# Kernel optimization log

Hardware: AMD Instinct MI355X
Metric: run time of the kernel (lower is better)

Reference implementation:

```python
import jax, jax.numpy as jnp
import numpy as np

HIDDEN = 256
HEADS = 8
DK = HIDDEN // HEADS
BH = 16  # bias_h_size
N = 2048
B = 1


def setup_inputs() -> dict:
    key = jax.random.key(0)
    ks = jax.random.split(key, 20)
    s = 0.02
    inp = {
        "int_chain_label": jax.random.randint(ks[0], (N, N), 0, 2, dtype=jnp.int32),
        "dist_map": jax.random.uniform(ks[1], (N, N), dtype=jnp.float32),
        "contact_map": jax.random.uniform(ks[2], (N, N), dtype=jnp.float32),
        "q": jax.random.normal(ks[3], (B, N, HIDDEN), dtype=jnp.float32),
        "k": jax.random.normal(ks[4], (B, N, HIDDEN), dtype=jnp.float32),
        "v": jax.random.normal(ks[5], (B, N, HIDDEN), dtype=jnp.float32),
        # projections
        "Wq": jax.random.normal(ks[6], (HIDDEN, HIDDEN), dtype=jnp.float32) * s,
        "bq": jnp.zeros((HIDDEN,), jnp.float32),
        "Wk": jax.random.normal(ks[7], (HIDDEN, HIDDEN), dtype=jnp.float32) * s,
        "bk": jnp.zeros((HIDDEN,), jnp.float32),
        "Wv": jax.random.normal(ks[8], (HIDDEN, HIDDEN), dtype=jnp.float32) * s,
        "bv": jnp.zeros((HIDDEN,), jnp.float32),
        "Wo": jax.random.normal(ks[9], (HIDDEN, HIDDEN), dtype=jnp.float32) * s,
        "bo": jnp.zeros((HIDDEN,), jnp.float32),
        # distance bias MLP: Linear(2, BH) -> Linear(BH, 1)
        "Wd1": jax.random.normal(ks[10], (2, BH), dtype=jnp.float32) * 0.5,
        "bd1": jnp.zeros((BH,), jnp.float32),
        "Wd2": jax.random.normal(ks[11], (BH, 1), dtype=jnp.float32) * 0.5,
        "bd2": jnp.zeros((1,), jnp.float32),
        # contact bias MLP
        "Wc1": jax.random.normal(ks[12], (2, BH), dtype=jnp.float32) * 0.5,
        "bc1": jnp.zeros((BH,), jnp.float32),
        "Wc2": jax.random.normal(ks[13], (BH, 1), dtype=jnp.float32) * 0.5,
        "bc2": jnp.zeros((1,), jnp.float32),
    }
    return inp


def _pair_bias(mp, label_f, W1, b1, W2, b2):
    # stack(map, label) -> [N,N,2]; two linears (no nonlinearity in original) -> [N,N]
    x = jnp.stack((mp, label_f), axis=-1)
    h = x @ W1 + b1                      # [N,N,BH]
    return (h @ W2 + b2)[..., 0]          # [N,N]


def reference(int_chain_label, dist_map, contact_map, q, k, v,
              Wq, bq, Wk, bk, Wv, bv, Wo, bo,
              Wd1, bd1, Wd2, bd2, Wc1, bc1, Wc2, bc2):
    label_f = int_chain_label.astype(jnp.float32)
    bias = (_pair_bias(dist_map, label_f, Wd1, bd1, Wd2, bd2)
            + _pair_bias(contact_map, label_f, Wc1, bc1, Wc2, bc2))  # [N,N]
    bias = bias[None, None]  # [1,1,N,N] broadcast over batch, heads

    b, n, _ = q.shape
    scale = DK ** -0.5
    qh = (q @ Wq + bq).reshape(b, n, HEADS, DK).transpose(0, 2, 1, 3) * scale  # [B,H,N,D]
    kh = (k @ Wk + bk).reshape(b, n, HEADS, DK).transpose(0, 2, 1, 3)
    vh = (v @ Wv + bv).reshape(b, n, HEADS, DK).transpose(0, 2, 1, 3)

    scores = jnp.einsum('bhnd,bhmd->bhnm', qh, kh) + bias  # [B,H,N,N]
    attn = jax.nn.softmax(scores, axis=-1)
    out = jnp.einsum('bhnm,bhmd->bhnd', attn, vh)           # [B,H,N,D]
    out = out.transpose(0, 2, 1, 3).reshape(b, n, HEADS * DK)
    return out @ Wo + bo
```

## Files before the change

kernel.cpp:

```cpp
#include <hip/hip_runtime.h>
#include <hip/hip_bf16.h>

#define SN 2048
#define HD 256
#define NHEAD 8
#define DK 32
#define BH 16

typedef __bf16 bf16;
typedef __bf16 bf16x8 __attribute__((ext_vector_type(8)));
typedef __bf16 bf16x4 __attribute__((ext_vector_type(4)));
typedef float f32x4 __attribute__((ext_vector_type(4)));
typedef int i32x4 __attribute__((ext_vector_type(4)));

__global__ void __launch_bounds__(256) prep_wt_kernel(
    const float* __restrict__ Wq, const float* __restrict__ Wk,
    const float* __restrict__ Wv, const float* __restrict__ Wo,
    bf16* __restrict__ wt)
{
    __shared__ bf16 tile[32][HD + 8];
    int bid = blockIdx.x;
    int t = threadIdx.x;
    const float* W = bid == 0 ? Wq : bid == 1 ? Wk : bid == 2 ? Wv : Wo;
    bf16* Wt = wt + bid * HD * HD;
    for (int r0 = 0; r0 < HD; r0 += 32) {
        #pragma unroll
        for (int i = 0; i < 32; i++) tile[i][t] = (bf16)W[(r0 + i) * HD + t];
        __syncthreads();
        #pragma unroll
        for (int i = 0; i < 32; i++) Wt[t * HD + r0 + i] = tile[i][t];
        __syncthreads();
    }
}

template<bool AF32, int MODE, bool OUTF32>
__device__ __forceinline__ void gemm_body(
    const void* __restrict__ Ap, const bf16* __restrict__ Wt,
    const float* __restrict__ bias, void* __restrict__ outp, int bid)
{
    int wave = threadIdx.x >> 6, lane = threadIdx.x & 63;
    int g = lane >> 4, qi = lane & 15;
    int mblk = bid & 31, nblk = bid >> 5;
    int m0 = mblk * 64 + wave * 16, n0 = nblk * 32;
    f32x4 acc0 = {0.f, 0.f, 0.f, 0.f}, acc1 = {0.f, 0.f, 0.f, 0.f};
    const bf16* W0 = Wt + (n0 + qi) * HD + 8 * g;
    const bf16* W1 = W0 + 16 * HD;
    #pragma unroll
    for (int ks = 0; ks < 8; ks++) {
        bf16x8 a;
        if constexpr (AF32) {
            const float* Ar = (const float*)Ap + (m0 + qi) * HD + 8 * g + ks * 32;
            f32x4 lo = *(const f32x4*)Ar;
            f32x4 hi = *(const f32x4*)(Ar + 4);
            #pragma unroll
            for (int e = 0; e < 4; e++) { a[e] = (bf16)lo[e]; a[4 + e] = (bf16)hi[e]; }
        } else {
            a = *(const bf16x8*)((const bf16*)Ap + (m0 + qi) * HD + 8 * g + ks * 32);
        }
        bf16x8 b0 = *(const bf16x8*)(W0 + ks * 32);
        bf16x8 b1 = *(const bf16x8*)(W1 + ks * 32);
        acc0 = __builtin_amdgcn_mfma_f32_16x16x32_bf16(a, b0, acc0, 0, 0, 0);
        acc1 = __builtin_amdgcn_mfma_f32_16x16x32_bf16(a, b1, acc1, 0, 0, 0);
    }
    float bv0 = bias[n0 + qi], bv1 = bias[n0 + 16 + qi];
    if constexpr (MODE == 0) {
        if constexpr (OUTF32) {
            float* out = (float*)outp;
            #pragma unroll
            for (int r = 0; r < 4; r++) {
                int m = m0 + 4 * g + r;
                out[m * HD + n0 + qi]      = acc0[r] + bv0;
                out[m * HD + n0 + 16 + qi] = acc1[r] + bv1;
            }
        } else {
            bf16* out = (bf16*)outp;
            #pragma unroll
            for (int r = 0; r < 4; r++) {
                int m = m0 + 4 * g + r;
                out[m * HD + n0 + qi]      = (bf16)(acc0[r] + bv0);
                out[m * HD + n0 + 16 + qi] = (bf16)(acc1[r] + bv1);
            }
        }
    } else {
        bf16* out = (bf16*)outp;
        bf16x4 v0, v1;
        #pragma unroll
        for (int r = 0; r < 4; r++) { v0[r] = (bf16)(acc0[r] + bv0); v1[r] = (bf16)(acc1[r] + bv1); }
        *(bf16x4*)(out + (n0 + qi) * SN + m0 + 4 * g)      = v0;
        *(bf16x4*)(out + (n0 + 16 + qi) * SN + m0 + 4 * g) = v1;
    }
}

__global__ void __launch_bounds__(256) qkv_kernel(
    const float* __restrict__ q, const float* __restrict__ k, const float* __restrict__ v,
    const bf16* __restrict__ wt,
    const float* __restrict__ bq, const float* __restrict__ bk, const float* __restrict__ bv,
    bf16* __restrict__ qh, bf16* __restrict__ kh, bf16* __restrict__ vt)
{
    int w = blockIdx.y;
    if (w == 0)      gemm_body<true, 0, false>(q, wt,               bq, qh, blockIdx.x);
    else if (w == 1) gemm_body<true, 0, false>(k, wt + HD * HD,     bk, kh, blockIdx.x);
    else             gemm_body<true, 1, false>(v, wt + 2 * HD * HD, bv, vt, blockIdx.x);
}

__global__ void __launch_bounds__(256) oproj_kernel(
    const bf16* __restrict__ A, const bf16* __restrict__ wt3,
    const float* __restrict__ bo, float* __restrict__ out)
{
    gemm_body<false, 0, true>(A, wt3, bo, out, blockIdx.x);
}

__global__ void __launch_bounds__(128) attn_kernel(
    const bf16* __restrict__ qh, const bf16* __restrict__ kh,
    const bf16* __restrict__ vt,
    const int* __restrict__ label, const float* __restrict__ dist,
    const float* __restrict__ contact,
    const float* __restrict__ Wd1, const float* __restrict__ bd1,
    const float* __restrict__ Wd2, const float* __restrict__ bd2,
    const float* __restrict__ Wc1, const float* __restrict__ bc1,
    const float* __restrict__ Wc2, const float* __restrict__ bc2,
    bf16* __restrict__ aout)
{
    int wave = threadIdx.x >> 6, lane = threadIdx.x & 63;
    int g = lane >> 4, qi = lane & 15;
    int h = blockIdx.x >> 6, qb = blockIdx.x & 63;
    int q0 = qb * 32 + wave * 16;

    float ad = 0.f, bld = 0.f, dd = bd2[0];
    #pragma unroll
    for (int j = 0; j < BH; j++) {
        float w2 = Wd2[j];
        ad  += Wd1[j] * w2;
        bld += Wd1[BH + j] * w2;
        dd  += bd1[j] * w2;
    }
    float ac = 0.f, blc = 0.f, dc = bc2[0];
    #pragma unroll
    for (int j = 0; j < BH; j++) {
        float w2 = Wc2[j];
        ac  += Wc1[j] * w2;
        blc += Wc1[BH + j] * w2;
        dc  += bc1[j] * w2;
    }
    float bl = bld + blc, dl = dd + dc;

    __shared__ bf16 plds[2][16][72];
    bf16 (*P)[72] = plds[wave];

    bf16x8 qf = *(const bf16x8*)(qh + (q0 + qi) * HD + h * DK + 8 * g);
    const bf16* kp  = kh + h * DK + 8 * g;
    const bf16* v0p = vt + (h * DK + qi) * SN + 8 * g;
    const bf16* v1p = v0p + 16 * SN;
    const float* dp = dist    + (q0 + qi) * SN + 4 * g;
    const float* cp = contact + (q0 + qi) * SN + 4 * g;
    const int*   lp = label   + (q0 + qi) * SN + 4 * g;

    const float scale = 0.17677669529663687f;
    float m = -1e30f, lsum = 0.f;
    f32x4 o0 = {0.f, 0.f, 0.f, 0.f}, o1 = {0.f, 0.f, 0.f, 0.f};

    for (int kt = 0; kt < 32; kt++) {
        int key0 = kt * 64;
        bf16x8 kf0 = *(const bf16x8*)(kp + (key0 +  0 + qi) * HD);
        bf16x8 kf1 = *(const bf16x8*)(kp + (key0 + 16 + qi) * HD);
        bf16x8 kf2 = *(const bf16x8*)(kp + (key0 + 32 + qi) * HD);
        bf16x8 kf3 = *(const bf16x8*)(kp + (key0 + 48 + qi) * HD);
        f32x4 dv0 = *(const f32x4*)(dp + key0 +  0), dv1 = *(const f32x4*)(dp + key0 + 16);
        f32x4 dv2 = *(const f32x4*)(dp + key0 + 32), dv3 = *(const f32x4*)(dp + key0 + 48);
        f32x4 cv0 = *(const f32x4*)(cp + key0 +  0), cv1 = *(const f32x4*)(cp + key0 + 16);
        f32x4 cv2 = *(const f32x4*)(cp + key0 + 32), cv3 = *(const f32x4*)(cp + key0 + 48);
        i32x4 lv0 = *(const i32x4*)(lp + key0 +  0), lv1 = *(const i32x4*)(lp + key0 + 16);
        i32x4 lv2 = *(const i32x4*)(lp + key0 + 32), lv3 = *(const i32x4*)(lp + key0 + 48);
        f32x4 zero = {0.f, 0.f, 0.f, 0.f};
        f32x4 s0 = __builtin_amdgcn_mfma_f32_16x16x32_bf16(kf0, qf, zero, 0, 0, 0);
        f32x4 s1 = __builtin_amdgcn_mfma_f32_16x16x32_bf16(kf1, qf, zero, 0, 0, 0);
        f32x4 s2 = __builtin_amdgcn_mfma_f32_16x16x32_bf16(kf2, qf, zero, 0, 0, 0);
        f32x4 s3 = __builtin_amdgcn_mfma_f32_16x16x32_bf16(kf3, qf, zero, 0, 0, 0);
        float x[16];
        #pragma unroll
        for (int r = 0; r < 4; r++) {
            float b0 = ad * dv0[r] + ac * cv0[r] + bl * (float)lv0[r] + dl;
            float b1 = ad * dv1[r] + ac * cv1[r] + bl * (float)lv1[r] + dl;
            float b2 = ad * dv2[r] + ac * cv2[r] + bl * (float)lv2[r] + dl;
            float b3 = ad * dv3[r] + ac * cv3[r] + bl * (float)lv3[r] + dl;
            x[r]      = s0[r] * scale + b0;
            x[4 + r]  = s1[r] * scale + b1;
            x[8 + r]  = s2[r] * scale + b2;
            x[12 + r] = s3[r] * scale + b3;
        }
        float tm = x[0];
        #pragma unroll
        for (int i = 1; i < 16; i++) tm = fmaxf(tm, x[i]);
        tm = fmaxf(tm, __shfl_xor(tm, 16));
        tm = fmaxf(tm, __shfl_xor(tm, 32));
        float mnew = fmaxf(m, tm);
        float f = __expf(m - mnew);
        float ps = 0.f;
        #pragma unroll
        for (int i = 0; i < 16; i++) { x[i] = __expf(x[i] - mnew); ps += x[i]; }
        ps += __shfl_xor(ps, 16);
        ps += __shfl_xor(ps, 32);
        lsum = lsum * f + ps;
        m = mnew;
        #pragma unroll
        for (int r = 0; r < 4; r++) { o0[r] *= f; o1[r] *= f; }
        #pragma unroll
        for (int s = 0; s < 4; s++) {
            bf16x4 pv;
            #pragma unroll
            for (int r = 0; r < 4; r++) pv[r] = (bf16)x[s * 4 + r];
            *(bf16x4*)(&P[qi][16 * s + 4 * g]) = pv;
        }
        __syncthreads();
        bf16x4 pa0 = *(const bf16x4*)(&P[qi][8 * g]);
        bf16x4 pa1 = *(const bf16x4*)(&P[qi][8 * g + 4]);
        bf16x4 pa2 = *(const bf16x4*)(&P[qi][32 + 8 * g]);
        bf16x4 pa3 = *(const bf16x4*)(&P[qi][32 + 8 * g + 4]);
        bf16x8 pb0 = __builtin_shufflevector(pa0, pa1, 0, 1, 2, 3, 4, 5, 6, 7);
        bf16x8 pb1 = __builtin_shufflevector(pa2, pa3, 0, 1, 2, 3, 4, 5, 6, 7);
        bf16x8 va00 = *(const bf16x8*)(v0p + key0);
        bf16x8 va01 = *(const bf16x8*)(v0p + key0 + 32);
        bf16x8 va10 = *(const bf16x8*)(v1p + key0);
        bf16x8 va11 = *(const bf16x8*)(v1p + key0 + 32);
        o0 = __builtin_amdgcn_mfma_f32_16x16x32_bf16(va00, pb0, o0, 0, 0, 0);
        o0 = __builtin_amdgcn_mfma_f32_16x16x32_bf16(va01, pb1, o0, 0, 0, 0);
        o1 = __builtin_amdgcn_mfma_f32_16x16x32_bf16(va10, pb0, o1, 0, 0, 0);
        o1 = __builtin_amdgcn_mfma_f32_16x16x32_bf16(va11, pb1, o1, 0, 0, 0);
        __syncthreads();
    }
    float inv = 1.f / lsum;
    bf16x4 r0, r1;
    #pragma unroll
    for (int r = 0; r < 4; r++) { r0[r] = (bf16)(o0[r] * inv); r1[r] = (bf16)(o1[r] * inv); }
    *(bf16x4*)(aout + (q0 + qi) * HD + h * DK + 4 * g)      = r0;
    *(bf16x4*)(aout + (q0 + qi) * HD + h * DK + 16 + 4 * g) = r1;
}

extern "C" void kernel_launch(void* const* d_in, const int* in_sizes, int n_in,
                              void* d_out, int out_size, void* d_ws, size_t ws_size,
                              hipStream_t stream)
{
    static const int expect[22] = {
        SN * SN, SN * SN, SN * SN,
        SN * HD, SN * HD, SN * HD,
        HD * HD, HD, HD * HD, HD,
        HD * HD, HD, HD * HD, HD,
        2 * BH, BH, BH, 1,
        2 * BH, BH, BH, 1
    };
    if (n_in != 22) return;
    for (int i = 0; i < 22; i++) if (in_sizes[i] != expect[i]) return;

    const int*   label   = (const int*)  d_in[0];
    const float* dist    = (const float*)d_in[1];
    const float* contact = (const float*)d_in[2];
    const float* q  = (const float*)d_in[3];
    const float* k  = (const float*)d_in[4];
    const float* v  = (const float*)d_in[5];
    const float* Wq = (const float*)d_in[6];  const float* bq = (const float*)d_in[7];
    const float* Wk = (const float*)d_in[8];  const float* bk = (const float*)d_in[9];
    const float* Wv = (const float*)d_in[10]; const float* bv = (const float*)d_in[11];
    const float* Wo = (const float*)d_in[12]; const float* bo = (const float*)d_in[13];
    const float* Wd1 = (const float*)d_in[14]; const float* bd1 = (const float*)d_in[15];
    const float* Wd2 = (const float*)d_in[16]; const float* bd2 = (const float*)d_in[17];
    const float* Wc1 = (const float*)d_in[18]; const float* bc1 = (const float*)d_in[19];
    const float* Wc2 = (const float*)d_in[20]; const float* bc2 = (const float*)d_in[21];

    char* ws = (char*)d_ws;
    bf16* qh   = (bf16*)(ws);
    bf16* kh   = (bf16*)(ws + (1u << 20));
    bf16* vt   = (bf16*)(ws + (2u << 20));
    bf16* aout = (bf16*)(ws + (3u << 20));
    bf16* wt   = (bf16*)(ws + (4u << 20));

    prep_wt_kernel<<<dim3(4), 256, 0, stream>>>(Wq, Wk, Wv, Wo, wt);

    qkv_kernel<<<dim3(256, 3), 256, 0, stream>>>(q, k, v, wt, bq, bk, bv, qh, kh, vt);

    attn_kernel<<<dim3(512), 128, 0, stream>>>(
        qh, kh, vt, label, dist, contact,
        Wd1, bd1, Wd2, bd2, Wc1, bc1, Wc2, bc2, aout);

    oproj_kernel<<<dim3(256), 256, 0, stream>>>(aout, wt + 3 * HD * HD, bo, (float*)d_out);
}
```

Before: 248.1 us.

## Split attention over key chunks with a separate combine kernel

The attention kernel now splits the key range into four chunks per (head, query block), which raises the grid from 512 to 2048 blocks. Each block writes partial outputs plus its running max and sum to workspace, and a new combine kernel merges them with log-sum-exp weights. The intra-wave __syncthreads are replaced with compiler memory barriers, since each wave uses its own LDS slice. The weight prep kernel is spread over 32 blocks, and the max reduction becomes a tree. This adds an extra launch and traffic for the partial results, and relies on LDS ordering within a wave without an explicit barrier.

```diff
diff --git a/kernel.cpp b/kernel.cpp
--- a/kernel.cpp
+++ b/kernel.cpp
@@ -6,6 +6,8 @@
 #define NHEAD 8
 #define DK 32
 #define BH 16
+#define KCH 4
+#define KTILES 8
 
 typedef __bf16 bf16;
 typedef __bf16 bf16x8 __attribute__((ext_vector_type(8)));
@@ -19,18 +21,16 @@
     bf16* __restrict__ wt)
 {
     __shared__ bf16 tile[32][HD + 8];
-    int bid = blockIdx.x;
+    int mat = blockIdx.x >> 3, rc = blockIdx.x & 7;
     int t = threadIdx.x;
-    const float* W = bid == 0 ? Wq : bid == 1 ? Wk : bid == 2 ? Wv : Wo;
-    bf16* Wt = wt + bid * HD * HD;
-    for (int r0 = 0; r0 < HD; r0 += 32) {
-        #pragma unroll
-        for (int i = 0; i < 32; i++) tile[i][t] = (bf16)W[(r0 + i) * HD + t];
-        __syncthreads();
-        #pragma unroll
-        for (int i = 0; i < 32; i++) Wt[t * HD + r0 + i] = tile[i][t];
-        __syncthreads();
-    }
+    const float* W = mat == 0 ? Wq : mat == 1 ? Wk : mat == 2 ? Wv : Wo;
+    bf16* Wt = wt + mat * HD * HD;
+    int r0 = rc * 32;
+    #pragma unroll
+    for (int i = 0; i < 32; i++) tile[i][t] = (bf16)W[(r0 + i) * HD + t];
+    __syncthreads();
+    #pragma unroll
+    for (int i = 0; i < 32; i++) Wt[t * HD + r0 + i] = tile[i][t];
 }
 
 template<bool AF32, int MODE, bool OUTF32>
@@ -119,12 +119,13 @@
     const float* __restrict__ Wd2, const float* __restrict__ bd2,
     const float* __restrict__ Wc1, const float* __restrict__ bc1,
     const float* __restrict__ Wc2, const float* __restrict__ bc2,
-    bf16* __restrict__ aout)
+    float* __restrict__ po, float* __restrict__ pm, float* __restrict__ pl)
 {
     int wave = threadIdx.x >> 6, lane = threadIdx.x & 63;
     int g = lane >> 4, qi = lane & 15;
-    int h = blockIdx.x >> 6, qb = blockIdx.x & 63;
+    int h = blockIdx.x >> 8, qb = (blockIdx.x >> 2) & 63, c = blockIdx.x & 3;
     int q0 = qb * 32 + wave * 16;
+    int kbase = c * (KTILES * 64);
 
     float ad = 0.f, bld = 0.f, dd = bd2[0];
     #pragma unroll
@@ -148,18 +149,18 @@
     bf16 (*P)[72] = plds[wave];
 
     bf16x8 qf = *(const bf16x8*)(qh + (q0 + qi) * HD + h * DK + 8 * g);
-    const bf16* kp  = kh + h * DK + 8 * g;
-    const bf16* v0p = vt + (h * DK + qi) * SN + 8 * g;
+    const bf16* kp  = kh + h * DK + 8 * g + kbase * HD;
+    const bf16* v0p = vt + (h * DK + qi) * SN + 8 * g + kbase;
     const bf16* v1p = v0p + 16 * SN;
-    const float* dp = dist    + (q0 + qi) * SN + 4 * g;
-    const float* cp = contact + (q0 + qi) * SN + 4 * g;
-    const int*   lp = label   + (q0 + qi) * SN + 4 * g;
+    const float* dp = dist    + (q0 + qi) * SN + 4 * g + kbase;
+    const float* cp = contact + (q0 + qi) * SN + 4 * g + kbase;
+    const int*   lp = label   + (q0 + qi) * SN + 4 * g + kbase;
 
     const float scale = 0.17677669529663687f;
     float m = -1e30f, lsum = 0.f;
     f32x4 o0 = {0.f, 0.f, 0.f, 0.f}, o1 = {0.f, 0.f, 0.f, 0.f};
 
-    for (int kt = 0; kt < 32; kt++) {
+    for (int kt = 0; kt < KTILES; kt++) {
         int key0 = kt * 64;
         bf16x8 kf0 = *(const bf16x8*)(kp + (key0 +  0 + qi) * HD);
         bf16x8 kf1 = *(const bf16x8*)(kp + (key0 + 16 + qi) * HD);
@@ -188,9 +189,12 @@
             x[8 + r]  = s2[r] * scale + b2;
             x[12 + r] = s3[r] * scale + b3;
         }
-        float tm = x[0];
-        #pragma unroll
-        for (int i = 1; i < 16; i++) tm = fmaxf(tm, x[i]);
+        float t0 = fmaxf(x[0], x[1]),  t1 = fmaxf(x[2], x[3]);
+        float t2 = fmaxf(x[4], x[5]),  t3 = fmaxf(x[6], x[7]);
+        float t4 = fmaxf(x[8], x[9]),  t5 = fmaxf(x[10], x[11]);
+        float t6 = fmaxf(x[12], x[13]), t7 = fmaxf(x[14], x[15]);
+        float tm = fmaxf(fmaxf(fmaxf(t0, t1), fmaxf(t2, t3)),
+                         fmaxf(fmaxf(t4, t5), fmaxf(t6, t7)));
         tm = fmaxf(tm, __shfl_xor(tm, 16));
         tm = fmaxf(tm, __shfl_xor(tm, 32));
         float mnew = fmaxf(m, tm);
@@ -211,11 +215,12 @@
             for (int r = 0; r < 4; r++) pv[r] = (bf16)x[s * 4 + r];
             *(bf16x4*)(&P[qi][16 * s + 4 * g]) = pv;
         }
-        __syncthreads();
+        asm volatile("" ::: "memory");
         bf16x4 pa0 = *(const bf16x4*)(&P[qi][8 * g]);
         bf16x4 pa1 = *(const bf16x4*)(&P[qi][8 * g + 4]);
         bf16x4 pa2 = *(const bf16x4*)(&P[qi][32 + 8 * g]);
         bf16x4 pa3 = *(const bf16x4*)(&P[qi][32 + 8 * g + 4]);
+        asm volatile("" ::: "memory");
         bf16x8 pb0 = __builtin_shufflevector(pa0, pa1, 0, 1, 2, 3, 4, 5, 6, 7);
         bf16x8 pb1 = __builtin_shufflevector(pa2, pa3, 0, 1, 2, 3, 4, 5, 6, 7);
         bf16x8 va00 = *(const bf16x8*)(v0p + key0);
@@ -226,14 +231,29 @@
         o0 = __builtin_amdgcn_mfma_f32_16x16x32_bf16(va01, pb1, o0, 0, 0, 0);
         o1 = __builtin_amdgcn_mfma_f32_16x16x32_bf16(va10, pb0, o1, 0, 0, 0);
         o1 = __builtin_amdgcn_mfma_f32_16x16x32_bf16(va11, pb1, o1, 0, 0, 0);
-        __syncthreads();
-    }
-    float inv = 1.f / lsum;
-    bf16x4 r0, r1;
-    #pragma unroll
-    for (int r = 0; r < 4; r++) { r0[r] = (bf16)(o0[r] * inv); r1[r] = (bf16)(o1[r] * inv); }
-    *(bf16x4*)(aout + (q0 + qi) * HD + h * DK + 4 * g)      = r0;
-    *(bf16x4*)(aout + (q0 + qi) * HD + h * DK + 16 + 4 * g) = r1;
+    }
+    int hq = h * SN + q0 + qi;
+    *(f32x4*)(po + (hq * KCH + c) * DK + 4 * g)      = o0;
+    *(f32x4*)(po + (hq * KCH + c) * DK + 16 + 4 * g) = o1;
+    if (g == 0) { pm[hq * KCH + c] = m; pl[hq * KCH + c] = lsum; }
+}
+
+__global__ void __launch_bounds__(256) combine_kernel(
+    const float* __restrict__ po, const float* __restrict__ pm,
+    const float* __restrict__ pl, bf16* __restrict__ aout)
+{
+    int idx = blockIdx.x * 256 + threadIdx.x;
+    int d = idx & (DK - 1), hq = idx >> 5;
+    int h = hq >> 11, qr = hq & (SN - 1);
+    f32x4 mv = *(const f32x4*)(pm + hq * KCH);
+    f32x4 lv = *(const f32x4*)(pl + hq * KCH);
+    float M = fmaxf(fmaxf(mv[0], mv[1]), fmaxf(mv[2], mv[3]));
+    float w0 = __expf(mv[0] - M), w1 = __expf(mv[1] - M);
+    float w2 = __expf(mv[2] - M), w3 = __expf(mv[3] - M);
+    float L = w0 * lv[0] + w1 * lv[1] + w2 * lv[2] + w3 * lv[3];
+    const float* p = po + hq * KCH * DK + d;
+    float o = w0 * p[0] + w1 * p[DK] + w2 * p[2 * DK] + w3 * p[3 * DK];
+    aout[qr * HD + h * DK + d] = (bf16)(o / L);
 }
 
 extern "C" void kernel_launch(void* const* d_in, const int* in_sizes, int n_in,
@@ -267,19 +287,24 @@
     const float* Wc2 = (const float*)d_in[20]; const float* bc2 = (const float*)d_in[21];
 
     char* ws = (char*)d_ws;
-    bf16* qh   = (bf16*)(ws);
-    bf16* kh   = (bf16*)(ws + (1u << 20));
-    bf16* vt   = (bf16*)(ws + (2u << 20));
-    bf16* aout = (bf16*)(ws + (3u << 20));
-    bf16* wt   = (bf16*)(ws + (4u << 20));
-
-    prep_wt_kernel<<<dim3(4), 256, 0, stream>>>(Wq, Wk, Wv, Wo, wt);
+    bf16*  qh   = (bf16*)(ws);
+    bf16*  kh   = (bf16*)(ws + (1u << 20));
+    bf16*  vt   = (bf16*)(ws + (2u << 20));
+    bf16*  aout = (bf16*)(ws + (3u << 20));
+    bf16*  wt   = (bf16*)(ws + (4u << 20));
+    float* po   = (float*)(ws + (5u << 20));
+    float* pm   = (float*)(ws + (13u << 20));
+    float* pl   = (float*)(ws + (13u << 20) + (256u << 10));
+
+    prep_wt_kernel<<<dim3(32), 256, 0, stream>>>(Wq, Wk, Wv, Wo, wt);
 
     qkv_kernel<<<dim3(256, 3), 256, 0, stream>>>(q, k, v, wt, bq, bk, bv, qh, kh, vt);
 
-    attn_kernel<<<dim3(512), 128, 0, stream>>>(
+    attn_kernel<<<dim3(NHEAD * 64 * KCH), 128, 0, stream>>>(
         qh, kh, vt, label, dist, contact,
-        Wd1, bd1, Wd2, bd2, Wc1, bc1, Wc2, bc2, aout);
+        Wd1, bd1, Wd2, bd2, Wc1, bc1, Wc2, bc2, po, pm, pl);
+
+    combine_kernel<<<dim3(NHEAD * SN * DK / 256), 256, 0, stream>>>(po, pm, pl, aout);
 
     oproj_kernel<<<dim3(256), 256, 0, stream>>>(aout, wt + 3 * HD * HD, bo, (float*)d_out);
 }
```

Measured after the change: 221.2 us. -10.8%, faster.
